# Optimization experiments

Hardware: AMD Instinct MI355X
Metric: run time of the kernel (lower is better)

Reference implementation:

```python
import jax, jax.numpy as jnp
import numpy as np

B, T, D_IN, D_H = 4, 8192, 512, 512


def log_g(x):
    # log of g(x) = where(x>=0, x+0.5, sigmoid(x))
    return jnp.where(x >= 0, jnp.log(jax.nn.relu(x) + 0.5), -jax.nn.softplus(-x))


def setup_inputs() -> dict:
    key = jax.random.key(0)
    ks = jax.random.split(key, 8)
    s = 1.0 / np.sqrt(D_IN)
    return {
        "x": jax.random.normal(ks[0], (B, T, D_IN), jnp.float32),
        "h_0": jax.random.uniform(ks[1], (B, 1, D_H), jnp.float32),
        "Wf": jax.random.uniform(ks[2], (D_H, D_IN), jnp.float32, -s, s),
        "bf": jax.random.uniform(ks[3], (D_H,), jnp.float32, -s, s),
        "Wi": jax.random.uniform(ks[4], (D_H, D_IN), jnp.float32, -s, s),
        "bi": jax.random.uniform(ks[5], (D_H,), jnp.float32, -s, s),
        "Wh": jax.random.uniform(ks[6], (D_H, D_IN), jnp.float32, -s, s),
        "bh": jax.random.uniform(ks[7], (D_H,), jnp.float32, -s, s),
    }


def reference(x, h_0, Wf, bf, Wi, bi, Wh, bh):
    # projections: (B, T, D_H)
    f_pre = jnp.einsum("bti,hi->bth", x, Wf) + bf
    i_pre = jnp.einsum("bti,hi->bth", x, Wi) + bi
    h_pre = jnp.einsum("bti,hi->bth", x, Wh) + bh

    diff = jax.nn.softplus(-f_pre) - jax.nn.softplus(-i_pre)
    log_f = -jax.nn.softplus(diff)   # log sigma-normalized forget gate
    log_i = -jax.nn.softplus(-diff)  # log input gate

    log_h0 = log_g(h_0)              # (B, 1, D_H)
    log_tilde_h = log_g(h_pre)       # (B, T, D_H)
    log_values = jnp.concatenate([log_h0, log_i + log_tilde_h], axis=1)  # (B, T+1, D_H)

    # parallel_scan_log: h_t = exp(a*_t + logcumsumexp(values - a*))
    a_star = jnp.pad(jnp.cumsum(log_f, axis=1), ((0, 0), (1, 0), (0, 0)))  # (B, T+1, D_H)
    log_h = a_star + jax.lax.cumlogsumexp(log_values - a_star, axis=1)
    return jnp.exp(log_h)[:, 1:]  # (B, T, D_H)
```

## Files before the change

kernel.cpp:

```cpp
#include <hip/hip_runtime.h>
#include <hip/hip_bf16.h>
#include <stdint.h>

#define T_SEQ 8192
#define BB    4
#define DH    512
#define DIN   512
#define M_TOT (BB*T_SEQ)
#define BM    128
#define BCH   64
#define BK    64
#define NKT   24
#define KS    1024
#define CHUNK_L 128
#define NCHUNK  64
#define NCH_TOT (BB*DH)
#define GRID_WG 2048
#define LDS_HALF 20480

#define XB_BLOCKS 8192
#define BM_BLOCKS 384

typedef __attribute__((ext_vector_type(4))) float f32x4;
typedef __attribute__((ext_vector_type(8))) short bf16x8;

__device__ __forceinline__ unsigned short f2bf_rne(float x){
  unsigned u = __float_as_uint(x);
  return (unsigned short)((u + 0x7FFFu + ((u >> 16) & 1u)) >> 16);
}
__device__ __forceinline__ float bf2f(unsigned short h){
  return __uint_as_float(((unsigned)h) << 16);
}
__device__ __forceinline__ void gld16(const void* g, void* l){
  __builtin_amdgcn_global_load_lds((const __attribute__((address_space(1))) unsigned*)g,
                                   (__attribute__((address_space(3))) unsigned*)l, 16, 0, 0);
}

__device__ __forceinline__ void split8_store(const float* src, unsigned short* dhi){
  float4 a = *(const float4*)src;
  float4 b = *(const float4*)(src + 4);
  float xs[8] = {a.x, a.y, a.z, a.w, b.x, b.y, b.z, b.w};
  unsigned short hi[8], lo[8];
#pragma unroll
  for (int e = 0; e < 8; ++e){
    hi[e] = f2bf_rne(xs[e]);
    lo[e] = f2bf_rne(xs[e] - bf2f(hi[e]));
  }
  uint4 ph, pl;
  ph.x = hi[0] | ((unsigned)hi[1] << 16); ph.y = hi[2] | ((unsigned)hi[3] << 16);
  ph.z = hi[4] | ((unsigned)hi[5] << 16); ph.w = hi[6] | ((unsigned)hi[7] << 16);
  pl.x = lo[0] | ((unsigned)lo[1] << 16); pl.y = lo[2] | ((unsigned)lo[3] << 16);
  pl.z = lo[4] | ((unsigned)lo[5] << 16); pl.w = lo[6] | ((unsigned)lo[7] << 16);
  *(uint4*)dhi = ph;
  *(uint4*)(dhi + 512) = pl;
}

__global__ void aug_build(const float* __restrict__ X,
                          const float* __restrict__ Wf, const float* __restrict__ Wi,
                          const float* __restrict__ Wh,
                          unsigned short* __restrict__ Xa, unsigned short* __restrict__ Bm,
                          int with_xa){
  int bx = blockIdx.x;
  if (with_xa && bx < XB_BLOCKS){
    int g = bx * 256 + threadIdx.x;
    int row  = g >> 6;
    int tile = (g >> 3) & 7;
    int clog = g & 7;
    int cphys = clog ^ (row & 7);
    split8_store(X + (size_t)row * DIN + tile * 64 + clog * 8,
                 Xa + (size_t)row * KS + tile * 64 + cphys * 8);
  } else {
    int g = (bx - (with_xa ? XB_BLOCKS : 0)) * 256 + threadIdx.x;
    int gate = g >> 15;
    int ch   = (g >> 6) & 511;
    int tile = (g >> 3) & 7;
    int clog = g & 7;
    const float* W = (gate == 0) ? Wf : ((gate == 1) ? Wi : Wh);
    int cphys = clog ^ (ch & 7);
    split8_store(W + (size_t)ch * DIN + tile * 64 + clog * 8,
                 Bm + (size_t)(gate * 512 + ch) * KS + tile * 64 + cphys * 8);
  }
}

__device__ __forceinline__ void gates_eval(float fp, float ip, float hp, float& fg, float& v){
  float zf = -fp, zi = -ip;
  float spf = fmaxf(zf, 0.f) + log1pf(expf(-fabsf(zf)));
  float spi = fmaxf(zi, 0.f) + log1pf(expf(-fabsf(zi)));
  float ef  = expf(spf - spi);
  fg = 1.f / (1.f + ef);
  float g = (hp >= 0.f) ? (hp + 0.5f) : (1.f / (1.f + expf(-hp)));
  v = (1.f - fg) * g;
}

__device__ __forceinline__ void gate_epilogue3(const f32x4 acc[4][3], int m0, int c0,
                                               int wm, int wn, int lr, int lg,
                                               const float* bfb, const float* bib, const float* bhb,
                                               float* Fw, float* Vw){
  int chan = c0 + wn * 16 + lr;
  float bfv = bfb[chan], biv = bib[chan], bhv = bhb[chan];
#pragma unroll
  for (int mi = 0; mi < 4; ++mi){
#pragma unroll
    for (int r = 0; r < 4; ++r){
      int bt = m0 + wm * 64 + mi * 16 + lg * 4 + r;
      float fg, v;
      gates_eval(acc[mi][0][r] + bfv, acc[mi][1][r] + biv, acc[mi][2][r] + bhv, fg, v);
      size_t idx = (size_t)bt * DH + chan;
      Fw[idx] = fg;
      Vw[idx] = v;
    }
  }
}

__launch_bounds__(512, 4)
__global__ void gemm_fast(const unsigned short* __restrict__ Xa, const unsigned short* __restrict__ Bm,
                          const float* __restrict__ bfb, const float* __restrict__ bib,
                          const float* __restrict__ bhb,
                          float* __restrict__ Fw, float* __restrict__ Vw,
                          float2* __restrict__ S){
  __shared__ unsigned short smem[2 * LDS_HALF];
  const int tid = threadIdx.x, wid = tid >> 6, lane = tid & 63;
  const int wg = (blockIdx.x & 7) * (GRID_WG / 8) + (blockIdx.x >> 3);
  const int m0 = (wg >> 3) * BM, c0 = (wg & 7) * BCH;
  const int wm = wid >> 2, wn = wid & 3, lr = lane & 15, lg = lane >> 4;

  const unsigned short* aS0 = Xa + (size_t)(m0 + (tid >> 3)) * KS + (tid & 7) * 8;
  const unsigned short* aS1 = aS0 + (size_t)64 * KS;
  const unsigned short* bS[3];
#pragma unroll
  for (int q = 0; q < 3; ++q){
    int ci = q * 512 + tid, row = ci >> 3, cp = ci & 7;
    bS[q] = Bm + (size_t)((row >> 6) * 512 + c0 + (row & 63)) * KS + cp * 8;
  }
  const int ldst = (tid & ~63) * 8;
  unsigned short* buf0 = smem;
  unsigned short* buf1 = smem + LDS_HALF;

  f32x4 acc[4][3];
#pragma unroll
  for (int a = 0; a < 4; ++a)
#pragma unroll
    for (int b = 0; b < 3; ++b) acc[a][b] = {0.f, 0.f, 0.f, 0.f};

  auto stage = [&](int kt, unsigned short* buf){
    const int aoff = (kt < 16 ? kt : kt - 16) * 64;
    const int boff = (kt < 8  ? kt : kt - 8 ) * 64;
    unsigned short* aD = buf + ldst;
    gld16(aS0 + aoff, aD);
    gld16(aS1 + aoff, aD + 4096);
    unsigned short* bD = buf + 8192 + ldst;
#pragma unroll
    for (int q = 0; q < 3; ++q) gld16(bS[q] + boff, bD + q * 4096);
  };

  auto compute = [&](const unsigned short* lA){
    const unsigned short* lB = lA + 8192;
#pragma unroll
    for (int kk = 0; kk < 2; ++kk){
      bf16x8 af[4], bfr[3];
#pragma unroll
      for (int mi = 0; mi < 4; ++mi){
        int row = wm * 64 + mi * 16 + lr;
        int ch  = (kk * 4 + lg) ^ (row & 7);
        af[mi] = *(const bf16x8*)(lA + row * 64 + ch * 8);
      }
#pragma unroll
      for (int j = 0; j < 3; ++j){
        int row = j * 64 + wn * 16 + lr;
        int ch  = (kk * 4 + lg) ^ (row & 7);
        bfr[j] = *(const bf16x8*)(lB + row * 64 + ch * 8);
      }
      __builtin_amdgcn_s_setprio(1);
#pragma unroll
      for (int mi = 0; mi < 4; ++mi)
#pragma unroll
        for (int j = 0; j < 3; ++j)
          acc[mi][j] = __builtin_amdgcn_mfma_f32_16x16x32_bf16(af[mi], bfr[j], acc[mi][j], 0, 0, 0);
      __builtin_amdgcn_s_setprio(0);
    }
  };

  stage(0, buf0);
  __syncthreads();
  for (int it = 0; it < NKT / 2; ++it){
    stage(2 * it + 1, buf1);
    compute(buf0);
    __syncthreads();
    if (2 * it + 2 < NKT) stage(2 * it + 2, buf0);
    compute(buf1);
    __syncthreads();
  }

  float2* pairs = (float2*)smem;
  float2* part4 = ((float2*)smem) + 64 * 32;
  const int chan_l = wn * 16 + lr;
  const int chan   = c0 + chan_l;
  {
    float bfv = bfb[chan], biv = bib[chan], bhv = bhb[chan];
#pragma unroll
    for (int mi = 0; mi < 4; ++mi){
      float F4 = 1.f, V4 = 0.f;
#pragma unroll
      for (int r = 0; r < 4; ++r){
        int bt = m0 + wm * 64 + mi * 16 + lg * 4 + r;
        float fg, v;
        gates_eval(acc[mi][0][r] + bfv, acc[mi][1][r] + biv, acc[mi][2][r] + bhv, fg, v);
        size_t idx = (size_t)bt * DH + chan;
        Fw[idx] = fg;
        Vw[idx] = v;
        F4 = fg * F4;
        V4 = fmaf(fg, V4, v);
      }
      pairs[chan_l * 32 + wm * 16 + mi * 4 + lg] = make_float2(F4, V4);
    }
  }
  __syncthreads();
  if (tid < 256){
    int cl = tid >> 2, q = tid & 3;
    float F = 1.f, V = 0.f;
#pragma unroll
    for (int i = 0; i < 8; ++i){
      float2 pr = pairs[cl * 32 + q * 8 + i];
      F = pr.x * F;
      V = fmaf(pr.x, V, pr.y);
    }
    part4[cl * 4 + q] = make_float2(F, V);
  }
  __syncthreads();
  if (tid < 64){
    float F = 1.f, V = 0.f;
#pragma unroll
    for (int i = 0; i < 4; ++i){
      float2 pr = part4[tid * 4 + i];
      F = pr.x * F;
      V = fmaf(pr.x, V, pr.y);
    }
    int b     = m0 >> 13;
    int chunk = (m0 & 8191) >> 7;
    S[chunk * NCH_TOT + b * DH + c0 + tid] = make_float2(F, V);
  }
}

__launch_bounds__(512, 2)
__global__ void gemm_slow(const float* __restrict__ X, const unsigned short* __restrict__ Bm,
                          const float* __restrict__ bfb, const float* __restrict__ bib,
                          const float* __restrict__ bhb,
                          float* __restrict__ Fw, float* __restrict__ Vw){
  __shared__ unsigned short smem[LDS_HALF];
  unsigned short* lA = smem;
  unsigned short* lB = smem + 8192;
  const int tid = threadIdx.x, wid = tid >> 6, lane = tid & 63;
  const int m0 = blockIdx.x * BM, c0 = blockIdx.y * BCH;
  const int wm = wid >> 2, wn = wid & 3, lr = lane & 15, lg = lane >> 4;

  const unsigned short* bS[3];
#pragma unroll
  for (int q = 0; q < 3; ++q){
    int ci = q * 512 + tid, row = ci >> 3, cp = ci & 7;
    bS[q] = Bm + (size_t)((row >> 6) * 512 + c0 + (row & 63)) * KS + cp * 8;
  }
  unsigned short* bD0 = lB + (size_t)(tid & ~63) * 8;

  f32x4 acc[4][3];
#pragma unroll
  for (int a = 0; a < 4; ++a)
#pragma unroll
    for (int b = 0; b < 3; ++b) acc[a][b] = {0.f, 0.f, 0.f, 0.f};

  for (int kt = 0; kt < NKT; ++kt){
    const bool losec = (kt >= 8 && kt < 16);
    const int  ko    = (kt < 8 ? kt : (kt < 16 ? kt - 8 : kt - 16)) * 64;
    const int  boff  = (kt < 8 ? kt : kt - 8) * 64;
    if (kt) __syncthreads();
#pragma unroll
    for (int q = 0; q < 2; ++q){
      int ci = q * 512 + tid, row = ci >> 3, kc = ci & 7;
      const float* src = X + (size_t)(m0 + row) * DIN + ko + kc * 8;
      float4 xa = *(const float4*)src;
      float4 xb = *(const float4*)(src + 4);
      float xs[8] = {xa.x, xa.y, xa.z, xa.w, xb.x, xb.y, xb.z, xb.w};
      unsigned short hs[8];
#pragma unroll
      for (int e = 0; e < 8; ++e){
        unsigned short h = f2bf_rne(xs[e]);
        hs[e] = losec ? f2bf_rne(xs[e] - bf2f(h)) : h;
      }
      uint4 pk;
      pk.x = hs[0] | ((unsigned)hs[1] << 16); pk.y = hs[2] | ((unsigned)hs[3] << 16);
      pk.z = hs[4] | ((unsigned)hs[5] << 16); pk.w = hs[6] | ((unsigned)hs[7] << 16);
      *(uint4*)(lA + row * 64 + ((kc ^ (row & 7)) * 8)) = pk;
    }
#pragma unroll
    for (int q = 0; q < 3; ++q) gld16(bS[q] + boff, bD0 + q * 4096);
    __syncthreads();
#pragma unroll
    for (int kk = 0; kk < 2; ++kk){
      bf16x8 af[4], bfr[3];
#pragma unroll
      for (int mi = 0; mi < 4; ++mi){
        int row = wm * 64 + mi * 16 + lr;
        int ch  = (kk * 4 + lg) ^ (row & 7);
        af[mi] = *(const bf16x8*)(lA + row * 64 + ch * 8);
      }
#pragma unroll
      for (int j = 0; j < 3; ++j){
        int row = j * 64 + wn * 16 + lr;
        int ch  = (kk * 4 + lg) ^ (row & 7);
        bfr[j] = *(const bf16x8*)(lB + row * 64 + ch * 8);
      }
#pragma unroll
      for (int mi = 0; mi < 4; ++mi)
#pragma unroll
        for (int j = 0; j < 3; ++j)
          acc[mi][j] = __builtin_amdgcn_mfma_f32_16x16x32_bf16(af[mi], bfr[j], acc[mi][j], 0, 0, 0);
    }
  }
  gate_epilogue3(acc, m0, c0, wm, wn, lr, lg, bfb, bib, bhb, Fw, Vw);
}

__global__ void scan_chunks(const float* __restrict__ Fw, const float* __restrict__ Vw,
                            float2* __restrict__ S){
  int bx = blockIdx.x;
  int chunk = bx >> 2, b = bx & 3;
  int ch4 = threadIdx.x * 4;
  size_t base = ((size_t)(b * T_SEQ + chunk * CHUNK_L)) * DH + ch4;
  float4 Fc = make_float4(1.f, 1.f, 1.f, 1.f);
  float4 Vc = make_float4(0.f, 0.f, 0.f, 0.f);
#pragma unroll 8
  for (int t = 0; t < CHUNK_L; ++t){
    float4 f = *(const float4*)(Fw + base + (size_t)t * DH);
    float4 v = *(const float4*)(Vw + base + (size_t)t * DH);
    Fc.x *= f.x; Fc.y *= f.y; Fc.z *= f.z; Fc.w *= f.w;
    Vc.x = fmaf(f.x, Vc.x, v.x); Vc.y = fmaf(f.y, Vc.y, v.y);
    Vc.z = fmaf(f.z, Vc.z, v.z); Vc.w = fmaf(f.w, Vc.w, v.w);
  }
  float2* s = S + (size_t)chunk * NCH_TOT + b * DH + ch4;
  s[0] = make_float2(Fc.x, Vc.x);
  s[1] = make_float2(Fc.y, Vc.y);
  s[2] = make_float2(Fc.z, Vc.z);
  s[3] = make_float2(Fc.w, Vc.w);
}

__global__ void scan_carry(const float2* __restrict__ S, const float* __restrict__ h0,
                           float* __restrict__ Hs){
  int cg = blockIdx.x * 256 + threadIdx.x;
  float hv = h0[cg];
  float h = (hv >= 0.f) ? (hv + 0.5f) : (1.f / (1.f + expf(-hv)));
  float2 s = S[cg];
#pragma unroll 16
  for (int k = 0; k < NCHUNK; ++k){
    float2 snext = (k + 1 < NCHUNK) ? S[(k + 1) * NCH_TOT + cg] : make_float2(0.f, 0.f);
    Hs[k * NCH_TOT + cg] = h;
    h = fmaf(s.x, h, s.y);
    s = snext;
  }
}

__global__ void scan_apply(const float* __restrict__ Fw, const float* Vw,
                           const float* __restrict__ Hs, float* out){
  int bx = blockIdx.x;
  int chunk = bx >> 2, b = bx & 3;
  int ch4 = threadIdx.x * 4;
  float4 h = *(const float4*)(Hs + (size_t)chunk * NCH_TOT + b * DH + ch4);
  size_t base = ((size_t)(b * T_SEQ + chunk * CHUNK_L)) * DH + ch4;
#pragma unroll 8
  for (int t = 0; t < CHUNK_L; ++t){
    size_t idx = base + (size_t)t * DH;
    float4 f = *(const float4*)(Fw + idx);
    float4 v = *(const float4*)(Vw + idx);
    h.x = fmaf(f.x, h.x, v.x); h.y = fmaf(f.y, h.y, v.y);
    h.z = fmaf(f.z, h.z, v.z); h.w = fmaf(f.w, h.w, v.w);
    *(float4*)(out + idx) = h;
  }
}

extern "C" void kernel_launch(void* const* d_in, const int* in_sizes, int n_in,
                              void* d_out, int out_size, void* d_ws, size_t ws_size,
                              hipStream_t stream){
  (void)in_sizes; (void)n_in; (void)out_size;
  const float* X  = (const float*)d_in[0];
  const float* h0 = (const float*)d_in[1];
  const float* Wf = (const float*)d_in[2];
  const float* bf = (const float*)d_in[3];
  const float* Wi = (const float*)d_in[4];
  const float* bi = (const float*)d_in[5];
  const float* Wh = (const float*)d_in[6];
  const float* bh = (const float*)d_in[7];

  constexpr size_t XA_B = (size_t)M_TOT * KS * 2;
  constexpr size_t F_B  = (size_t)M_TOT * DH * 4;
  constexpr size_t S_B  = (size_t)NCHUNK * NCH_TOT * 8;
  constexpr size_t H_B  = (size_t)NCHUNK * NCH_TOT * 4;
  constexpr size_t BMB  = (size_t)3 * 512 * KS * 2;
  const bool fast = ws_size >= XA_B + F_B + S_B + H_B + BMB;

  char* ws = (char*)d_ws;
  float* Vw  = (float*)d_out;
  float* out = (float*)d_out;

  if (fast){
    unsigned short* Xa  = (unsigned short*)ws;
    float*          Fw  = (float*)(ws + XA_B);
    float2*         S   = (float2*)(ws + XA_B + F_B);
    float*          Hs  = (float*)(ws + XA_B + F_B + S_B);
    unsigned short* Bmw = (unsigned short*)(ws + XA_B + F_B + S_B + H_B);
    aug_build <<<XB_BLOCKS + BM_BLOCKS, 256, 0, stream>>>(X, Wf, Wi, Wh, Xa, Bmw, 1);
    gemm_fast <<<GRID_WG, 512, 0, stream>>>(Xa, Bmw, bf, bi, bh, Fw, Vw, S);
    scan_carry <<<8, 256, 0, stream>>>(S, h0, Hs);
    scan_apply <<<256, 128, 0, stream>>>(Fw, Vw, Hs, out);
  } else {
    float*          Fw  = (float*)ws;
    float2*         S   = (float2*)(ws + F_B);
    float*          Hs  = (float*)(ws + F_B + S_B);
    unsigned short* Bmw = (unsigned short*)(ws + F_B + S_B + H_B);
    aug_build <<<BM_BLOCKS, 256, 0, stream>>>(X, Wf, Wi, Wh, nullptr, Bmw, 0);
    gemm_slow <<<dim3(M_TOT / BM, DH / BCH), 512, 0, stream>>>(X, Bmw, bf, bi, bh, Fw, Vw);
    scan_chunks<<<256, 128, 0, stream>>>(Fw, Vw, S);
    scan_carry <<<8, 256, 0, stream>>>(S, h0, Hs);
    scan_apply <<<256, 128, 0, stream>>>(Fw, Vw, Hs, out);
  }
}
```

Baseline: 411.3 us.

## Drop third split-bf16 GEMM pass and simplify chunk reduction

Cuts the K-loop from 24 to 16 tiles by dropping one of the three hi/lo bf16 product terms (likely the lo-weight × hi-activation term), which reduces MFMA work and global loads by a third. The chunk-summary reduction now goes from the per-thread partials straight to one pass over 32 entries with a padded stride, removing one barrier and one LDS stage. The dropped error-compensation term lowers the precision of the fp32 emulation and may push the output past tolerance.

Measured after the change: 376.1 us. 8.6% less time.

```diff
diff --git a/kernel.cpp b/kernel.cpp
--- a/kernel.cpp
+++ b/kernel.cpp
@@ -10,7 +10,7 @@
 #define BM    128
 #define BCH   64
 #define BK    64
-#define NKT   24
+#define NKT   16
 #define KS    1024
 #define CHUNK_L 128
 #define NCHUNK  64
@@ -143,8 +143,8 @@
     for (int b = 0; b < 3; ++b) acc[a][b] = {0.f, 0.f, 0.f, 0.f};
 
   auto stage = [&](int kt, unsigned short* buf){
-    const int aoff = (kt < 16 ? kt : kt - 16) * 64;
-    const int boff = (kt < 8  ? kt : kt - 8 ) * 64;
+    const int aoff = kt * 64;
+    const int boff = (kt & 7) * 64;
     unsigned short* aD = buf + ldst;
     gld16(aS0 + aoff, aD);
     gld16(aS1 + aoff, aD + 4096);
@@ -192,7 +192,6 @@
   }
 
   float2* pairs = (float2*)smem;
-  float2* part4 = ((float2*)smem) + 64 * 32;
   const int chan_l = wn * 16 + lr;
   const int chan   = c0 + chan_l;
   {
@@ -211,27 +210,15 @@
         F4 = fg * F4;
         V4 = fmaf(fg, V4, v);
       }
-      pairs[chan_l * 32 + wm * 16 + mi * 4 + lg] = make_float2(F4, V4);
-    }
-  }
-  __syncthreads();
-  if (tid < 256){
-    int cl = tid >> 2, q = tid & 3;
-    float F = 1.f, V = 0.f;
-#pragma unroll
-    for (int i = 0; i < 8; ++i){
-      float2 pr = pairs[cl * 32 + q * 8 + i];
-      F = pr.x * F;
-      V = fmaf(pr.x, V, pr.y);
-    }
-    part4[cl * 4 + q] = make_float2(F, V);
+      pairs[(wm * 16 + mi * 4 + lg) * 65 + chan_l] = make_float2(F4, V4);
+    }
   }
   __syncthreads();
   if (tid < 64){
     float F = 1.f, V = 0.f;
-#pragma unroll
-    for (int i = 0; i < 4; ++i){
-      float2 pr = part4[tid * 4 + i];
+#pragma unroll 8
+    for (int p = 0; p < 32; ++p){
+      float2 pr = pairs[p * 65 + tid];
       F = pr.x * F;
       V = fmaf(pr.x, V, pr.y);
     }
@@ -268,9 +255,9 @@
     for (int b = 0; b < 3; ++b) acc[a][b] = {0.f, 0.f, 0.f, 0.f};
 
   for (int kt = 0; kt < NKT; ++kt){
-    const bool losec = (kt >= 8 && kt < 16);
-    const int  ko    = (kt < 8 ? kt : (kt < 16 ? kt - 8 : kt - 16)) * 64;
-    const int  boff  = (kt < 8 ? kt : kt - 8) * 64;
+    const bool losec = (kt >= 8);
+    const int  ko    = (kt & 7) * 64;
+    const int  boff  = (kt & 7) * 64;
     if (kt) __syncthreads();
 #pragma unroll
     for (int q = 0; q < 2; ++q){
```
